# Optimization experiments

Hardware: AMD Instinct MI355X
Metric: run time of the kernel (lower is better)

## Reference

```python
import jax, jax.numpy as jnp
import numpy as np

BN_EPS = 1e-5


def setup_inputs() -> dict:
    key = jax.random.key(0)
    k1, k2, k3 = jax.random.split(key, 3)
    B, T, I, H = 64, 2048, 128, 128
    x = jax.random.normal(k1, (B, T, I), dtype=jnp.float32)
    W = jax.random.normal(k2, (H, I), dtype=jnp.float32) * (1.0 / np.sqrt(I))
    # orthogonal recurrent matrix, as in nn.init.orthogonal_
    V = jnp.linalg.qr(jax.random.normal(k3, (H, H), dtype=jnp.float32))[0]
    gamma = jnp.ones((H,), dtype=jnp.float32)
    beta = jnp.zeros((H,), dtype=jnp.float32)
    return {"x": x, "W": W, "V": V, "gamma": gamma, "beta": beta}


def reference(x, W, V, gamma, beta):
    B, T, H = x.shape[0], x.shape[1], W.shape[0]
    # feedforward projection: [B,T,I] @ [H,I]^T -> [B,T,H]
    Wx = jnp.einsum('bti,hi->bth', x, W)
    # batchnorm (training mode) over flattened (B*T, H)
    flat = Wx.reshape(B * T, H)
    mean = jnp.mean(flat, axis=0)
    var = jnp.var(flat, axis=0)
    Wx = ((flat - mean) * jax.lax.rsqrt(var + BN_EPS) * gamma + beta).reshape(B, T, H)
    # sequential recurrence: yt = sigmoid(Wx_t + yt @ V^T)
    Vt = V.T

    def step(yt, wx_t):
        yt = jax.nn.sigmoid(wx_t + yt @ Vt)
        return yt, yt

    y0 = jnp.zeros((B, H), dtype=Wx.dtype)
    _, ys = jax.lax.scan(step, y0, jnp.swapaxes(Wx, 0, 1))  # ys: [T,B,H]
    return jnp.swapaxes(ys, 0, 1)  # [B,T,H]
```

## Files before the change

kernel.cpp:

```cpp
#include <hip/hip_runtime.h>
#include <cstdint>
#include <cstddef>

#define N_ROWS 131072
#define T_LEN 2048
#define B_BATCH 64
#define H_DIM 128
#define GEMM_GRID 1024
#define WND 8
#define LOG2E 1.4426950408889634f

typedef _Float16 half2_t __attribute__((ext_vector_type(2)));
typedef _Float16 half8_t __attribute__((ext_vector_type(8)));
typedef float f32x4_t __attribute__((ext_vector_type(4)));
typedef int int2_t __attribute__((ext_vector_type(2)));

__device__ __forceinline__ float dpp_xor1(float x) {
  int i = __float_as_int(x);
  return __int_as_float(__builtin_amdgcn_update_dpp(i, i, 0xB1, 0xF, 0xF, true));
}
__device__ __forceinline__ float dpp_xor2(float x) {
  int i = __float_as_int(x);
  return __int_as_float(__builtin_amdgcn_update_dpp(i, i, 0x4E, 0xF, 0xF, true));
}
__device__ __forceinline__ float dpp_mirror8(float x) {
  int i = __float_as_int(x);
  return __int_as_float(__builtin_amdgcn_update_dpp(i, i, 0x141, 0xF, 0xF, true));
}

__device__ __forceinline__ float permlane16_sum(float x) {
  int i = __float_as_int(x);
  int2_t r = __builtin_amdgcn_permlane16_swap(i, i, false, false);
  return __int_as_float(r.x) + __int_as_float(r.y);
}
__device__ __forceinline__ float permlane32_sum(float x) {
  int i = __float_as_int(x);
  int2_t r = __builtin_amdgcn_permlane32_swap(i, i, false, false);
  return __int_as_float(r.x) + __int_as_float(r.y);
}

__device__ __forceinline__ float sigmoid2_fast(float spp) {
  return __builtin_amdgcn_rcpf(1.0f + __builtin_amdgcn_exp2f(spp));
}

__global__ __launch_bounds__(256) void gemm_bn_kernel(
    const float* __restrict__ x, const float* __restrict__ W,
    float* __restrict__ Wx, float* __restrict__ stats)
{
  const int tid  = threadIdx.x;
  const int lane = tid & 63;
  const int wv   = tid >> 6;
  const int l15  = lane & 15;
  const int kg   = lane >> 4;
  const int r0   = blockIdx.x * 128;

  half8_t Bf[2][4];
#pragma unroll
  for (int n = 0; n < 2; ++n) {
    const int col = wv * 32 + n * 16 + l15;
    const float* wp = W + (size_t)col * H_DIM;
#pragma unroll
    for (int k = 0; k < 4; ++k) {
      const float* w8 = wp + k * 32 + kg * 8;
      half8_t b;
#pragma unroll
      for (int i = 0; i < 8; ++i) b[i] = (_Float16)w8[i];
      Bf[n][k] = b;
    }
  }

  __shared__ __align__(16) _Float16 xs[128 * 128];
  {
    const int row = tid >> 1;
    const int hf  = tid & 1;
    const float* xp = x + (size_t)(r0 + row) * H_DIM + hf * 64;
    const int swz = (row & 7) << 4;
    char* base = reinterpret_cast<char*>(xs) + row * 256;
#pragma unroll
    for (int c = 0; c < 8; ++c) {
      float4 v0 = *reinterpret_cast<const float4*>(xp + c * 8);
      float4 v1 = *reinterpret_cast<const float4*>(xp + c * 8 + 4);
      half8_t h;
      h[0] = (_Float16)v0.x; h[1] = (_Float16)v0.y;
      h[2] = (_Float16)v0.z; h[3] = (_Float16)v0.w;
      h[4] = (_Float16)v1.x; h[5] = (_Float16)v1.y;
      h[6] = (_Float16)v1.z; h[7] = (_Float16)v1.w;
      const int X = hf * 128 + c * 16;
      *reinterpret_cast<half8_t*>(base + (X ^ swz)) = h;
    }
  }
  __syncthreads();

  f32x4_t C[8][2];
#pragma unroll
  for (int m = 0; m < 8; ++m)
#pragma unroll
    for (int n = 0; n < 2; ++n)
      C[m][n] = (f32x4_t){0.f, 0.f, 0.f, 0.f};

#pragma unroll
  for (int m = 0; m < 8; ++m) {
    const int row = m * 16 + l15;
    const char* rbase = reinterpret_cast<const char*>(xs) + row * 256;
    const int swz = (row & 7) << 4;
#pragma unroll
    for (int k = 0; k < 4; ++k) {
      const int X = k * 64 + kg * 16;
      half8_t a = *reinterpret_cast<const half8_t*>(rbase + (X ^ swz));
      C[m][0] = __builtin_amdgcn_mfma_f32_16x16x32_f16(a, Bf[0][k], C[m][0], 0, 0, 0);
      C[m][1] = __builtin_amdgcn_mfma_f32_16x16x32_f16(a, Bf[1][k], C[m][1], 0, 0, 0);
    }
  }

  float sum0 = 0.f, sq0 = 0.f, sum1 = 0.f, sq1 = 0.f;
#pragma unroll
  for (int m = 0; m < 8; ++m) {
#pragma unroll
    for (int j = 0; j < 4; ++j) {
      const int row = r0 + m * 16 + kg * 4 + j;
      const float v0 = C[m][0][j];
      const float v1 = C[m][1][j];
      Wx[(size_t)row * H_DIM + wv * 32 + l15]      = v0;
      Wx[(size_t)row * H_DIM + wv * 32 + 16 + l15] = v1;
      sum0 += v0; sq0 = fmaf(v0, v0, sq0);
      sum1 += v1; sq1 = fmaf(v1, v1, sq1);
    }
  }
  float s0 = permlane32_sum(permlane16_sum(sum0));
  float q0 = permlane32_sum(permlane16_sum(sq0));
  float s1 = permlane32_sum(permlane16_sum(sum1));
  float q1 = permlane32_sum(permlane16_sum(sq1));
  if (lane < 16) {
    atomicAdd(&stats[wv * 32 + lane],              s0);
    atomicAdd(&stats[H_DIM + wv * 32 + lane],      q0);
    atomicAdd(&stats[wv * 32 + 16 + lane],         s1);
    atomicAdd(&stats[H_DIM + wv * 32 + 16 + lane], q1);
  }
}

__global__ void bn_finalize_kernel(float* ws, const float* __restrict__ gamma,
                                   const float* __restrict__ beta)
{
  const int h = threadIdx.x;
  const float invN = 1.0f / (float)N_ROWS;
  float mean = ws[h] * invN;
  float e2   = ws[H_DIM + h] * invN;
  float var  = e2 - mean * mean;
  float scl  = gamma[h] * rsqrtf(var + 1e-5f);
  ws[2 * H_DIM + h] = scl;
  ws[3 * H_DIM + h] = beta[h] - mean * scl;
}

__global__ __launch_bounds__(256) void rnn_kernel(
    const float* __restrict__ V, float* __restrict__ out,
    const float* __restrict__ ws)
{
  const int tid = threadIdx.x;
  const int hq = tid >> 3;
  const int l7 = tid & 7;
  const int g  = (l7 & 3) ^ (3 * ((l7 >> 2) & 1));
  const int h_own = hq + (g << 5);
  const bool wr = (tid & 4) == 0;

  half2_t Vh[4][8];
#pragma unroll
  for (int j = 0; j < 4; ++j) {
    const int hrow = hq + (((unsigned)(j ^ g)) << 5);
    const float* vp = V + (size_t)hrow * H_DIM + (l7 << 4);
#pragma unroll
    for (int i = 0; i < 8; ++i) {
      half2_t h;
      h.x = (_Float16)(-LOG2E * vp[2 * i]);
      h.y = (_Float16)(-LOG2E * vp[2 * i + 1]);
      Vh[j][i] = h;
    }
  }
  const float scl2 = ws[2 * H_DIM + h_own] * (-LOG2E);
  const float shf2 = ws[3 * H_DIM + h_own] * (-LOG2E);

  __shared__ __align__(16) _Float16 ylds[2][H_DIM];

  float* outb = out + (size_t)blockIdx.x * T_LEN * H_DIM;

  if (tid < H_DIM) { ylds[0][tid] = (_Float16)0.f; ylds[1][tid] = (_Float16)0.f; }

  float wxp[WND];
  if (wr) {
#pragma unroll
    for (int u = 0; u < WND; ++u)
      wxp[u] = fmaf(outb[(size_t)u * H_DIM + h_own], scl2, shf2);
  } else {
#pragma unroll
    for (int u = 0; u < WND; ++u) wxp[u] = 0.f;
  }
  __syncthreads();

  float yreg[WND];

  for (int w = 0; w < T_LEN; w += WND) {
    const bool more = (w + WND < T_LEN);
    float wxn[WND];
    if (more && wr) {
#pragma unroll
      for (int u = 0; u < WND; ++u)
        wxn[u] = outb[(size_t)(w + WND + u) * H_DIM + h_own];
    } else {
#pragma unroll
      for (int u = 0; u < WND; ++u) wxn[u] = 0.f;
    }

#pragma unroll
    for (int u = 0; u < WND; ++u) {
      const int t = w + u;
      const uint4* yv = reinterpret_cast<const uint4*>(&ylds[t & 1][l7 << 4]);
      uint4 w0 = yv[0], w1 = yv[1];
      half2_t y2[8];
      y2[0] = __builtin_bit_cast(half2_t, w0.x);
      y2[1] = __builtin_bit_cast(half2_t, w0.y);
      y2[2] = __builtin_bit_cast(half2_t, w0.z);
      y2[3] = __builtin_bit_cast(half2_t, w0.w);
      y2[4] = __builtin_bit_cast(half2_t, w1.x);
      y2[5] = __builtin_bit_cast(half2_t, w1.y);
      y2[6] = __builtin_bit_cast(half2_t, w1.z);
      y2[7] = __builtin_bit_cast(half2_t, w1.w);

      float a0 = 0.f, a1 = 0.f, a2 = 0.f, a3 = 0.f;
#pragma unroll
      for (int i = 0; i < 8; ++i) {
        a0 = __builtin_amdgcn_fdot2(y2[i], Vh[0][i], a0, false);
        a1 = __builtin_amdgcn_fdot2(y2[i], Vh[1][i], a1, false);
        a2 = __builtin_amdgcn_fdot2(y2[i], Vh[2][i], a2, false);
        a3 = __builtin_amdgcn_fdot2(y2[i], Vh[3][i], a3, false);
      }
      float b0 = a0 + dpp_xor1(a1);
      float b1 = a2 + dpp_xor1(a3);
      float c  = b0 + dpp_xor2(b1);
      float red = c + dpp_mirror8(c);
      const float spp = red + wxp[u];
      const float y = sigmoid2_fast(spp);
      if (wr) ylds[(t & 1) ^ 1][h_own] = (_Float16)y;
      yreg[u] = y;
      asm volatile("s_waitcnt lgkmcnt(0)\n\ts_barrier" ::: "memory");
    }

    if (wr) {
#pragma unroll
      for (int u = 0; u < WND; ++u)
        outb[(size_t)(w + u) * H_DIM + h_own] = yreg[u];
    }
#pragma unroll
    for (int u = 0; u < WND; ++u) wxp[u] = fmaf(wxn[u], scl2, shf2);
  }
}

extern "C" void kernel_launch(void* const* d_in, const int* in_sizes, int n_in,
                              void* d_out, int out_size, void* d_ws, size_t ws_size,
                              hipStream_t stream)
{
  (void)in_sizes; (void)n_in; (void)out_size; (void)ws_size;
  const float* x     = (const float*)d_in[0];
  const float* W     = (const float*)d_in[1];
  const float* V     = (const float*)d_in[2];
  const float* gamma = (const float*)d_in[3];
  const float* beta  = (const float*)d_in[4];
  float* out = (float*)d_out;
  float* ws  = (float*)d_ws;

  hipMemsetAsync(ws, 0, 2 * H_DIM * sizeof(float), stream);
  gemm_bn_kernel<<<GEMM_GRID, 256, 0, stream>>>(x, W, out, ws);
  bn_finalize_kernel<<<1, H_DIM, 0, stream>>>(ws, gamma, beta);
  rnn_kernel<<<B_BATCH, 256, 0, stream>>>(V, out, ws);
}
```

Measured before the change: 519.2 us.

## Batch 16 sequences per block and use MFMA for the recurrent matvec

Replaces the per-sequence recurrence kernel (one block per batch element, fdot2 with DPP reductions) with a kernel where each block handles 16 batch rows. The recurrent step becomes a 16x128 by 128x128 product done with f16 MFMA instructions, using swizzled LDS for the hidden state. Only 4 blocks run instead of 64, which trades many parallel CUs for fewer, denser steps. The serial critical path per step now includes MFMA latency chains and strided output stores across 16 sequences.

```diff
diff --git a/kernel.cpp b/kernel.cpp
--- a/kernel.cpp
+++ b/kernel.cpp
@@ -7,26 +7,15 @@
 #define B_BATCH 64
 #define H_DIM 128
 #define GEMM_GRID 1024
-#define WND 8
+#define G_BATCH 16
+#define RNN_BLOCKS (B_BATCH / G_BATCH)
+#define RWND 4
 #define LOG2E 1.4426950408889634f
 
 typedef _Float16 half2_t __attribute__((ext_vector_type(2)));
 typedef _Float16 half8_t __attribute__((ext_vector_type(8)));
 typedef float f32x4_t __attribute__((ext_vector_type(4)));
 typedef int int2_t __attribute__((ext_vector_type(2)));
-
-__device__ __forceinline__ float dpp_xor1(float x) {
-  int i = __float_as_int(x);
-  return __int_as_float(__builtin_amdgcn_update_dpp(i, i, 0xB1, 0xF, 0xF, true));
-}
-__device__ __forceinline__ float dpp_xor2(float x) {
-  int i = __float_as_int(x);
-  return __int_as_float(__builtin_amdgcn_update_dpp(i, i, 0x4E, 0xF, 0xF, true));
-}
-__device__ __forceinline__ float dpp_mirror8(float x) {
-  int i = __float_as_int(x);
-  return __int_as_float(__builtin_amdgcn_update_dpp(i, i, 0x141, 0xF, 0xF, true));
-}
 
 __device__ __forceinline__ float permlane16_sum(float x) {
   int i = __float_as_int(x);
@@ -151,105 +140,127 @@
   ws[3 * H_DIM + h] = beta[h] - mean * scl;
 }
 
-__global__ __launch_bounds__(256) void rnn_kernel(
+__global__ __launch_bounds__(256) void rnn_mfma_kernel(
     const float* __restrict__ V, float* __restrict__ out,
     const float* __restrict__ ws)
 {
-  const int tid = threadIdx.x;
-  const int hq = tid >> 3;
-  const int l7 = tid & 7;
-  const int g  = (l7 & 3) ^ (3 * ((l7 >> 2) & 1));
-  const int h_own = hq + (g << 5);
-  const bool wr = (tid & 4) == 0;
-
-  half2_t Vh[4][8];
-#pragma unroll
-  for (int j = 0; j < 4; ++j) {
-    const int hrow = hq + (((unsigned)(j ^ g)) << 5);
-    const float* vp = V + (size_t)hrow * H_DIM + (l7 << 4);
-#pragma unroll
-    for (int i = 0; i < 8; ++i) {
-      half2_t h;
-      h.x = (_Float16)(-LOG2E * vp[2 * i]);
-      h.y = (_Float16)(-LOG2E * vp[2 * i + 1]);
-      Vh[j][i] = h;
-    }
-  }
-  const float scl2 = ws[2 * H_DIM + h_own] * (-LOG2E);
-  const float shf2 = ws[3 * H_DIM + h_own] * (-LOG2E);
-
-  __shared__ __align__(16) _Float16 ylds[2][H_DIM];
-
-  float* outb = out + (size_t)blockIdx.x * T_LEN * H_DIM;
-
-  if (tid < H_DIM) { ylds[0][tid] = (_Float16)0.f; ylds[1][tid] = (_Float16)0.f; }
-
-  float wxp[WND];
-  if (wr) {
-#pragma unroll
-    for (int u = 0; u < WND; ++u)
-      wxp[u] = fmaf(outb[(size_t)u * H_DIM + h_own], scl2, shf2);
-  } else {
-#pragma unroll
-    for (int u = 0; u < WND; ++u) wxp[u] = 0.f;
-  }
+  const int tid  = threadIdx.x;
+  const int lane = tid & 63;
+  const int wv   = tid >> 6;
+  const int n15  = lane & 15;
+  const int kg   = lane >> 4;
+
+  const int col0 = wv * 32 + n15;
+  const int col1 = col0 + 16;
+
+  half8_t Bf[2][4];
+#pragma unroll
+  for (int nt = 0; nt < 2; ++nt) {
+    const int col = nt ? col1 : col0;
+    const float* vp = V + (size_t)col * H_DIM;
+#pragma unroll
+    for (int ks = 0; ks < 4; ++ks) {
+      const float* v8 = vp + ks * 32 + kg * 8;
+      half8_t b;
+#pragma unroll
+      for (int i = 0; i < 8; ++i) b[i] = (_Float16)(-LOG2E * v8[i]);
+      Bf[nt][ks] = b;
+    }
+  }
+  float scl[2], shf[2];
+  scl[0] = ws[2 * H_DIM + col0] * (-LOG2E);
+  shf[0] = ws[3 * H_DIM + col0] * (-LOG2E);
+  scl[1] = ws[2 * H_DIM + col1] * (-LOG2E);
+  shf[1] = ws[3 * H_DIM + col1] * (-LOG2E);
+
+  __shared__ __align__(16) _Float16 ylds[2 * G_BATCH * H_DIM];
+  float* outb = out + (size_t)blockIdx.x * G_BATCH * T_LEN * H_DIM;
+
+  {
+    half8_t z = {};
+    char* zb = reinterpret_cast<char*>(ylds) + tid * 32;
+    *reinterpret_cast<half8_t*>(zb)      = z;
+    *reinterpret_cast<half8_t*>(zb + 16) = z;
+  }
+
+  float wxp[RWND][2][4];
+#pragma unroll
+  for (int u = 0; u < RWND; ++u)
+#pragma unroll
+    for (int nt = 0; nt < 2; ++nt)
+#pragma unroll
+      for (int j = 0; j < 4; ++j) {
+        const int col = nt ? col1 : col0;
+        float r = outb[((size_t)(kg * 4 + j) * T_LEN + u) * H_DIM + col];
+        wxp[u][nt][j] = fmaf(r, scl[nt], shf[nt]);
+      }
   __syncthreads();
 
-  float yreg[WND];
-
-  for (int w = 0; w < T_LEN; w += WND) {
-    const bool more = (w + WND < T_LEN);
-    float wxn[WND];
-    if (more && wr) {
-#pragma unroll
-      for (int u = 0; u < WND; ++u)
-        wxn[u] = outb[(size_t)(w + WND + u) * H_DIM + h_own];
-    } else {
-#pragma unroll
-      for (int u = 0; u < WND; ++u) wxn[u] = 0.f;
-    }
-
-#pragma unroll
-    for (int u = 0; u < WND; ++u) {
+  const int rsw = (n15 & 7) << 4;
+  const char* ybase = reinterpret_cast<const char*>(ylds);
+  char* ybase_w = reinterpret_cast<char*>(ylds);
+
+  for (int w = 0; w < T_LEN; w += RWND) {
+    const bool more = (w + RWND < T_LEN);
+    float wxn[RWND][2][4];
+    if (more) {
+#pragma unroll
+      for (int u = 0; u < RWND; ++u)
+#pragma unroll
+        for (int nt = 0; nt < 2; ++nt)
+#pragma unroll
+          for (int j = 0; j < 4; ++j) {
+            const int col = nt ? col1 : col0;
+            wxn[u][nt][j] =
+                outb[((size_t)(kg * 4 + j) * T_LEN + (w + RWND + u)) * H_DIM + col];
+          }
+    }
+
+#pragma unroll
+    for (int u = 0; u < RWND; ++u) {
       const int t = w + u;
-      const uint4* yv = reinterpret_cast<const uint4*>(&ylds[t & 1][l7 << 4]);
-      uint4 w0 = yv[0], w1 = yv[1];
-      half2_t y2[8];
-      y2[0] = __builtin_bit_cast(half2_t, w0.x);
-      y2[1] = __builtin_bit_cast(half2_t, w0.y);
-      y2[2] = __builtin_bit_cast(half2_t, w0.z);
-      y2[3] = __builtin_bit_cast(half2_t, w0.w);
-      y2[4] = __builtin_bit_cast(half2_t, w1.x);
-      y2[5] = __builtin_bit_cast(half2_t, w1.y);
-      y2[6] = __builtin_bit_cast(half2_t, w1.z);
-      y2[7] = __builtin_bit_cast(half2_t, w1.w);
-
-      float a0 = 0.f, a1 = 0.f, a2 = 0.f, a3 = 0.f;
-#pragma unroll
-      for (int i = 0; i < 8; ++i) {
-        a0 = __builtin_amdgcn_fdot2(y2[i], Vh[0][i], a0, false);
-        a1 = __builtin_amdgcn_fdot2(y2[i], Vh[1][i], a1, false);
-        a2 = __builtin_amdgcn_fdot2(y2[i], Vh[2][i], a2, false);
-        a3 = __builtin_amdgcn_fdot2(y2[i], Vh[3][i], a3, false);
+      const int cur = t & 1;
+      const char* rb = ybase + cur * 4096 + n15 * 256;
+      half8_t a0 = *reinterpret_cast<const half8_t*>(rb + ((0 * 64 + kg * 16) ^ rsw));
+      half8_t a1 = *reinterpret_cast<const half8_t*>(rb + ((1 * 64 + kg * 16) ^ rsw));
+      half8_t a2 = *reinterpret_cast<const half8_t*>(rb + ((2 * 64 + kg * 16) ^ rsw));
+      half8_t a3 = *reinterpret_cast<const half8_t*>(rb + ((3 * 64 + kg * 16) ^ rsw));
+
+      f32x4_t C0 = {wxp[u][0][0], wxp[u][0][1], wxp[u][0][2], wxp[u][0][3]};
+      f32x4_t C1 = {wxp[u][1][0], wxp[u][1][1], wxp[u][1][2], wxp[u][1][3]};
+      C0 = __builtin_amdgcn_mfma_f32_16x16x32_f16(a0, Bf[0][0], C0, 0, 0, 0);
+      C1 = __builtin_amdgcn_mfma_f32_16x16x32_f16(a0, Bf[1][0], C1, 0, 0, 0);
+      C0 = __builtin_amdgcn_mfma_f32_16x16x32_f16(a1, Bf[0][1], C0, 0, 0, 0);
+      C1 = __builtin_amdgcn_mfma_f32_16x16x32_f16(a1, Bf[1][1], C1, 0, 0, 0);
+      C0 = __builtin_amdgcn_mfma_f32_16x16x32_f16(a2, Bf[0][2], C0, 0, 0, 0);
+      C1 = __builtin_amdgcn_mfma_f32_16x16x32_f16(a2, Bf[1][2], C1, 0, 0, 0);
+      C0 = __builtin_amdgcn_mfma_f32_16x16x32_f16(a3, Bf[0][3], C0, 0, 0, 0);
+      C1 = __builtin_amdgcn_mfma_f32_16x16x32_f16(a3, Bf[1][3], C1, 0, 0, 0);
+
+      char* wb = ybase_w + (cur ^ 1) * 4096;
+#pragma unroll
+      for (int j = 0; j < 4; ++j) {
+        const int row = kg * 4 + j;
+        const int wsw = (row & 7) << 4;
+        const float y0 = sigmoid2_fast(C0[j]);
+        const float y1 = sigmoid2_fast(C1[j]);
+        *reinterpret_cast<_Float16*>(wb + row * 256 + ((col0 * 2) ^ wsw)) = (_Float16)y0;
+        *reinterpret_cast<_Float16*>(wb + row * 256 + ((col1 * 2) ^ wsw)) = (_Float16)y1;
+        outb[((size_t)row * T_LEN + t) * H_DIM + col0] = y0;
+        outb[((size_t)row * T_LEN + t) * H_DIM + col1] = y1;
       }
-      float b0 = a0 + dpp_xor1(a1);
-      float b1 = a2 + dpp_xor1(a3);
-      float c  = b0 + dpp_xor2(b1);
-      float red = c + dpp_mirror8(c);
-      const float spp = red + wxp[u];
-      const float y = sigmoid2_fast(spp);
-      if (wr) ylds[(t & 1) ^ 1][h_own] = (_Float16)y;
-      yreg[u] = y;
       asm volatile("s_waitcnt lgkmcnt(0)\n\ts_barrier" ::: "memory");
     }
 
-    if (wr) {
-#pragma unroll
-      for (int u = 0; u < WND; ++u)
-        outb[(size_t)(w + u) * H_DIM + h_own] = yreg[u];
-    }
-#pragma unroll
-    for (int u = 0; u < WND; ++u) wxp[u] = fmaf(wxn[u], scl2, shf2);
+    if (more) {
+#pragma unroll
+      for (int u = 0; u < RWND; ++u)
+#pragma unroll
+        for (int nt = 0; nt < 2; ++nt)
+#pragma unroll
+          for (int j = 0; j < 4; ++j)
+            wxp[u][nt][j] = fmaf(wxn[u][nt][j], scl[nt], shf[nt]);
+    }
   }
 }
 
@@ -269,5 +280,5 @@
   hipMemsetAsync(ws, 0, 2 * H_DIM * sizeof(float), stream);
   gemm_bn_kernel<<<GEMM_GRID, 256, 0, stream>>>(x, W, out, ws);
   bn_finalize_kernel<<<1, H_DIM, 0, stream>>>(ws, gamma, beta);
-  rnn_kernel<<<B_BATCH, 256, 0, stream>>>(V, out, ws);
-}
+  rnn_mfma_kernel<<<RNN_BLOCKS, 256, 0, stream>>>(V, out, ws);
+}
```

New measurement: 929.8 us. 1.79x slower.
